# Performance work log

Measured on AMD Instinct MI355X. Metric: run time of the kernel, lower is better.

## Reference

```python
import jax, jax.numpy as jnp
import numpy as np

B, SEED, GEN = 32, 128, 384
IN, H, OUT = 171, 1024, 171


def setup_inputs() -> dict:
    key = jax.random.key(0)
    ks = jax.random.split(key, 16)
    s = 0.05
    w = lambda k, shape: (jax.random.normal(k, shape, jnp.float32) * s)
    inp = {
        "seed_seq": jax.random.normal(ks[0], (B, SEED, IN), jnp.float32),
        "Wih1": w(ks[1], (4 * H, IN)),  "Whh1": w(ks[2], (4 * H, H)),
        "bih1": w(ks[3], (4 * H,)),     "bhh1": w(ks[4], (4 * H,)),
        "Wih2": w(ks[5], (4 * H, H)),   "Whh2": w(ks[6], (4 * H, H)),
        "bih2": w(ks[7], (4 * H,)),     "bhh2": w(ks[8], (4 * H,)),
        "Wih3": w(ks[9], (4 * H, H)),   "Whh3": w(ks[10], (4 * H, H)),
        "bih3": w(ks[11], (4 * H,)),    "bhh3": w(ks[12], (4 * H,)),
        "Wdec": w(ks[13], (OUT, H)),    "bdec": w(ks[14], (OUT,)),
        "gen_len": GEN,
    }
    return inp


def _lstm_cell(x, h, c, Wih, Whh, bih, bhh):
    # PyTorch LSTMCell: gate order i, f, g, o
    gates = x @ Wih.T + bih + h @ Whh.T + bhh  # [B, 4H]
    i, f, g, o = jnp.split(gates, 4, axis=-1)
    c_new = jax.nn.sigmoid(f) * c + jax.nn.sigmoid(i) * jnp.tanh(g)
    h_new = jax.nn.sigmoid(o) * jnp.tanh(c_new)
    return h_new, c_new


def reference(seed_seq, Wih1, Whh1, bih1, bhh1, Wih2, Whh2, bih2, bhh2,
              Wih3, Whh3, bih3, bhh3, Wdec, bdec, gen_len):
    batch = seed_seq.shape[0]
    hsz = Whh1.shape[1]
    z = jnp.zeros((batch, hsz), seed_seq.dtype)

    def step(state, x):
        h1, c1, h2, c2, h3, c3 = state
        h1, c1 = _lstm_cell(x, h1, c1, Wih1, Whh1, bih1, bhh1)
        h2, c2 = _lstm_cell(h1, h2, c2, Wih2, Whh2, bih2, bhh2)
        h3, c3 = _lstm_cell(h2, h3, c3, Wih3, Whh3, bih3, bhh3)
        out = h3 @ Wdec.T + bdec
        return (h1, c1, h2, c2, h3, c3), out

    # conditioning (seed) phase: scan over time-major seed sequence
    state0 = (z, z, z, z, z, z)
    state, seed_outs = jax.lax.scan(step, state0, jnp.swapaxes(seed_seq, 0, 1))

    def gen_step(carry, _):
        cur, st = carry
        st, out = step(st, cur)
        return (out, st), out

    _, gen_outs = jax.lax.scan(gen_step, (seed_outs[-1], state), None, length=gen_len)

    outs = jnp.concatenate([seed_outs, gen_outs], axis=0)  # [T, B, OUT]
    return jnp.swapaxes(outs, 0, 1)  # [B, T, OUT]
```

## Files before the change

kernel.cpp:

```cpp
#include <hip/hip_runtime.h>
#include <hip/hip_bf16.h>
#include <math.h>

#define NB    32
#define NSEED 128
#define NTT   512
#define NIN   171
#define NINP  192
#define NH    1024
#define NG    4096
#define NOUT  171
#define NOUTP 176
#define NWG   256

typedef unsigned short u16;
typedef unsigned int u32;
typedef __attribute__((ext_vector_type(8))) short bf16x8;
typedef __attribute__((ext_vector_type(4))) float f32x4;

__device__ __host__ inline u16 f2bf(float x) {
  union { float f; unsigned u; } v; v.f = x;
  unsigned r = v.u + 0x7FFFu + ((v.u >> 16) & 1u);
  return (u16)(r >> 16);
}

__global__ void pack_mat(const float* __restrict__ src, u16* __restrict__ dst, int ktiles) {
  int id = blockIdx.x * 256 + threadIdx.x;
  int total = ktiles * 256 * 64;
  if (id >= total) return;
  int lane = id & 63;
  int nt = (id >> 6) & 255;
  int kt = id >> 14;
  int c = lane & 15, q = lane >> 4;
  int r = (c & 3) * 1024 + nt * 4 + (c >> 2);
  int K = ktiles * 32;
  const float* s = src + (size_t)r * K + kt * 32 + q * 8;
  __attribute__((aligned(16))) u16 o[8];
#pragma unroll
  for (int j = 0; j < 8; ++j) o[j] = f2bf(s[j]);
  *(bf16x8*)(dst + (size_t)id * 8) = *(const bf16x8*)o;
}

__global__ void pack_wih1(const float* __restrict__ src, u16* __restrict__ dst) {
  int id = blockIdx.x * 256 + threadIdx.x;
  if (id >= 6 * 256 * 64) return;
  int lane = id & 63;
  int nt = (id >> 6) & 255;
  int kt = id >> 14;
  int c = lane & 15, q = lane >> 4;
  int r = (c & 3) * 1024 + nt * 4 + (c >> 2);
  int k0 = kt * 32 + q * 8;
  __attribute__((aligned(16))) u16 o[8];
#pragma unroll
  for (int j = 0; j < 8; ++j) {
    int k = k0 + j;
    o[j] = (k < NIN) ? f2bf(src[(size_t)r * NIN + k]) : (u16)0;
  }
  *(bf16x8*)(dst + (size_t)id * 8) = *(const bf16x8*)o;
}

__global__ void pack_wdec(const float* __restrict__ src, u16* __restrict__ dst) {
  int id = blockIdx.x * 256 + threadIdx.x;
  if (id >= 32 * 11 * 64) return;
  int lane = id & 63;
  int nt = (id >> 6) % 11;
  int kt = (id >> 6) / 11;
  int c = lane & 15, q = lane >> 4;
  int r = nt * 16 + c;
  int k0 = kt * 32 + q * 8;
  __attribute__((aligned(16))) u16 o[8];
#pragma unroll
  for (int j = 0; j < 8; ++j) {
    o[j] = (r < NOUT) ? f2bf(src[(size_t)r * NH + k0 + j]) : (u16)0;
  }
  *(bf16x8*)(dst + (size_t)id * 8) = *(const bf16x8*)o;
}

__global__ void pack_seed(const float* __restrict__ src, u16* __restrict__ dst) {
  int id = blockIdx.x * 256 + threadIdx.x;
  if (id >= NSEED * NB * NINP) return;
  int kp = id % NINP;
  int b = (id / NINP) % NB;
  int t = id / (NINP * NB);
  float v = (kp < NIN) ? src[((size_t)b * NSEED + t) * NIN + kp] : 0.f;
  dst[id] = f2bf(v);
}

__global__ void wfuse_kernel(const float* __restrict__ wih1, const float* __restrict__ wdec,
                             float* __restrict__ tmp) {
  int n = blockIdx.x;
  int k = blockIdx.y * 256 + threadIdx.x;
  const float* wr = wih1 + (size_t)n * NIN;
  float s = 0.f;
  for (int i = 0; i < NIN; ++i) s += wr[i] * wdec[(size_t)i * NH + k];
  tmp[(size_t)n * NH + k] = s;
}

__global__ void prep_bias(const float* bih1, const float* bhh1, const float* bih2, const float* bhh2,
                          const float* bih3, const float* bhh3, const float* __restrict__ wih1,
                          const float* __restrict__ bdec_in,
                          float* b1s, float* b1g, float* b2, float* b3, float* bdecp,
                          int* __restrict__ flags) {
  int n = blockIdx.x * 256 + threadIdx.x;
  if (n >= NG) return;
  int wgi = n >> 4, c = n & 15;
  int r = (c & 3) * 1024 + wgi * 4 + (c >> 2);
  float v1 = bih1[r] + bhh1[r];
  b1s[n] = v1;
  float bf = 0.f;
  for (int i = 0; i < NIN; ++i) bf += wih1[(size_t)r * NIN + i] * bdec_in[i];
  b1g[n] = v1 + bf;
  b2[n] = bih2[r] + bhh2[r];
  b3[n] = bih3[r] + bhh3[r];
  if (n < NOUTP) bdecp[n] = (n < NOUT) ? bdec_in[n] : 0.f;
  if (n < NWG) flags[n] = 0;
}

__device__ __forceinline__ float fsig(float x) {
  return __builtin_amdgcn_rcpf(1.f + __expf(-x));
}
__device__ __forceinline__ float ftanh(float x) {
  return 1.f - 2.f * __builtin_amdgcn_rcpf(1.f + __expf(2.f * x));
}

#define MFMA_BF16 __builtin_amdgcn_mfma_f32_16x16x32_bf16

__device__ __forceinline__ void mm32_lds(f32x4& d0, f32x4& d1, const u16* wl,
                                         const u16* __restrict__ x, int wv, int lane) {
  int m = lane & 15, q = lane >> 4;
  const u16* xa = x + m * NH + q * 8 + wv * 32;
  const u16* xb = xa + 16 * NH;
  const u16* wb = wl + lane * 8;
  bf16x8 w[8], a0[8], a1[8];
#pragma unroll
  for (int i = 0; i < 8; ++i) w[i] = *(const bf16x8*)(wb + (size_t)(wv + 4 * i) * 512);
#pragma unroll
  for (int i = 0; i < 8; ++i) {
    a0[i] = *(const bf16x8*)(xa + i * 128);
    a1[i] = *(const bf16x8*)(xb + i * 128);
  }
#pragma unroll
  for (int i = 0; i < 8; ++i) {
    d0 = MFMA_BF16(a0[i], w[i], d0, 0, 0, 0);
    d1 = MFMA_BF16(a1[i], w[i], d1, 0, 0, 0);
  }
}

__device__ __forceinline__ void mm32_glb(f32x4& d0, f32x4& d1, const u16* __restrict__ wgb,
                                         const u16* __restrict__ x, int wv, int lane) {
  int m = lane & 15, q = lane >> 4;
  const u16* xa = x + m * NH + q * 8 + wv * 32;
  const u16* xb = xa + 16 * NH;
  const u16* wb = wgb + lane * 8;
  bf16x8 w[8], a0[8], a1[8];
#pragma unroll
  for (int i = 0; i < 8; ++i) w[i] = *(const bf16x8*)(wb + (size_t)(wv + 4 * i) * 131072);
#pragma unroll
  for (int i = 0; i < 8; ++i) {
    a0[i] = *(const bf16x8*)(xa + i * 128);
    a1[i] = *(const bf16x8*)(xb + i * 128);
  }
#pragma unroll
  for (int i = 0; i < 8; ++i) {
    d0 = MFMA_BF16(a0[i], w[i], d0, 0, 0, 0);
    d1 = MFMA_BF16(a1[i], w[i], d1, 0, 0, 0);
  }
}

__device__ __forceinline__ void mm6_glb(f32x4& d0, f32x4& d1, const u16* __restrict__ wbase,
                                        const u16* __restrict__ x, int wv, int lane) {
  int m = lane & 15, q = lane >> 4;
  const u16* xa = x + m * NINP + q * 8;
  const u16* xb = xa + 16 * NINP;
  const u16* wb = wbase + lane * 8;
#pragma unroll
  for (int i = 0; i < 2; ++i) {
    int kt = wv + 4 * i;
    if (kt >= 6) break;
    bf16x8 w = *(const bf16x8*)(wb + (size_t)kt * 131072);
    bf16x8 a0 = *(const bf16x8*)(xa + kt * 32);
    bf16x8 a1 = *(const bf16x8*)(xb + kt * 32);
    d0 = MFMA_BF16(a0, w, d0, 0, 0, 0);
    d1 = MFMA_BF16(a1, w, d1, 0, 0, 0);
  }
}

__global__ __launch_bounds__(256, 1) void lstm_main(
    const u16* __restrict__ whh1, const u16* __restrict__ whh2, const u16* __restrict__ whh3,
    const u16* __restrict__ wih2, const u16* __restrict__ wih3,
    const u16* __restrict__ wfuse, const u16* __restrict__ wih1,
    const u16* __restrict__ seedp,
    u16* __restrict__ h1h, u16* __restrict__ h2h, u16* __restrict__ h3h,
    const float* __restrict__ b1s, const float* __restrict__ b1g,
    const float* __restrict__ b2, const float* __restrict__ b3,
    int* __restrict__ flags)
{
  __shared__ u16  wlds[3 * 16384];
  __shared__ float red[4][64][8];
  __shared__ float gbuf[32][16];
  __shared__ float cst[3][32][4];

  int wg = blockIdx.x;
  int tid = threadIdx.x;
  int wv = tid >> 6, lane = tid & 63;

  {
    const u16* srcs[3] = { wih2 + (size_t)wg * 512, wih3 + (size_t)wg * 512,
                           wfuse + (size_t)wg * 512 };
#pragma unroll
    for (int m = 0; m < 3; ++m) {
      for (int i = tid; i < 2048; i += 256) {
        int kt = i >> 6, ln = i & 63;
        *(bf16x8*)&wlds[m * 16384 + (kt * 64 + ln) * 8] =
            *(const bf16x8*)(srcs[m] + ((size_t)kt * 16384 + ln) * 8);
      }
    }
    float* cp = &cst[0][0][0];
    for (int i = tid; i < 3 * 32 * 4; i += 256) cp[i] = 0.f;
  }
  __syncthreads();

  int c0 = tid & 15;
  float bv_s  = b1s[wg * 16 + c0];
  float bv_g  = b1g[wg * 16 + c0];
  float bv_2  = b2 [wg * 16 + c0];
  float bv_3  = b3 [wg * 16 + c0];

  const u16* whhg[3] = { whh1 + (size_t)wg * 512, whh2 + (size_t)wg * 512,
                         whh3 + (size_t)wg * 512 };
  const u16* wih1g = wih1 + (size_t)wg * 512;

  int ep = 0;
  for (int t = 0; t < NTT; ++t) {
    for (int l = 0; l < 3; ++l) {
      f32x4 d0 = {0.f, 0.f, 0.f, 0.f}, d1 = {0.f, 0.f, 0.f, 0.f};
      bool isseed = (t < NSEED);

      if (l == 0 && isseed)
        mm6_glb(d0, d1, wih1g, seedp + (size_t)t * NB * NINP, wv, lane);
      if (t > 0) {
        const u16* hs = (l == 0) ? h1h + (size_t)(t - 1) * NB * NH
                     : (l == 1) ? h2h + (size_t)(t - 1) * NB * NH
                                : h3h + (size_t)(t - 1) * NB * NH;
        mm32_glb(d0, d1, whhg[l], hs, wv, lane);
      }

      bool skipwait = (l == 0 && isseed);
      if (ep > 0 && !skipwait) {
        if (tid < 64) {
          const int* fp = flags + (tid << 2);
          for (;;) {
            int f0 = __hip_atomic_load(fp + 0, __ATOMIC_RELAXED, __HIP_MEMORY_SCOPE_AGENT);
            int f1 = __hip_atomic_load(fp + 1, __ATOMIC_RELAXED, __HIP_MEMORY_SCOPE_AGENT);
            int f2 = __hip_atomic_load(fp + 2, __ATOMIC_RELAXED, __HIP_MEMORY_SCOPE_AGENT);
            int f3 = __hip_atomic_load(fp + 3, __ATOMIC_RELAXED, __HIP_MEMORY_SCOPE_AGENT);
            int mn = min(min(f0, f1), min(f2, f3));
            if (__all(mn >= ep)) break;
            __builtin_amdgcn_s_sleep(1);
          }
        }
        __syncthreads();
      }

      if (l == 0) {
        if (!isseed)
          mm32_lds(d0, d1, &wlds[2 * 16384], h3h + (size_t)(t - 1) * NB * NH, wv, lane);
      } else {
        const u16* xs = (l == 1) ? h1h + (size_t)t * NB * NH
                                 : h2h + (size_t)t * NB * NH;
        mm32_lds(d0, d1, &wlds[(l - 1) * 16384], xs, wv, lane);
      }

#pragma unroll
      for (int r = 0; r < 4; ++r) { red[wv][lane][r] = d0[r]; red[wv][lane][4 + r] = d1[r]; }
      __syncthreads();
      {
        int c = tid & 15, brow = tid >> 4;
        float bv = (l == 0) ? (isseed ? bv_s : bv_g) : (l == 1) ? bv_2 : bv_3;
        int srcl = ((brow >> 2) << 4) | c;
#pragma unroll
        for (int mt = 0; mt < 2; ++mt) {
          int b = brow + mt * 16;
          int idx = mt * 4 + (brow & 3);
          gbuf[b][c] = red[0][srcl][idx] + red[1][srcl][idx] +
                       red[2][srcl][idx] + red[3][srcl][idx] + bv;
        }
      }
      __syncthreads();

      if (tid < 128) {
        int b = tid & 31, jl = tid >> 5;
        float gi = gbuf[b][jl * 4 + 0], gf = gbuf[b][jl * 4 + 1];
        float gg = gbuf[b][jl * 4 + 2], go = gbuf[b][jl * 4 + 3];
        float si = fsig(gi);
        float sf = fsig(gf);
        float so = fsig(go);
        float cn = sf * cst[l][b][jl] + si * ftanh(gg);
        cst[l][b][jl] = cn;
        float hn = so * ftanh(cn);
        unsigned hv = (unsigned)f2bf(hn);
        unsigned other = (unsigned)__shfl_xor((int)hv, 32, 64);
        if (lane < 32) {
          unsigned val = hv | (other << 16);
          int w01 = tid >> 6;
          u16* hdst = (l == 0) ? h1h + (size_t)t * NB * NH
                    : (l == 1) ? h2h + (size_t)t * NB * NH
                               : h3h + (size_t)t * NB * NH;
          u32* hp = (u32*)hdst + (size_t)b * 512 + wg * 2 + w01;
          __hip_atomic_store(hp, val, __ATOMIC_RELAXED, __HIP_MEMORY_SCOPE_AGENT);
        }
      }

      __syncthreads();
      ++ep;
      if (tid == 0)
        __hip_atomic_store(&flags[wg], ep, __ATOMIC_RELAXED, __HIP_MEMORY_SCOPE_AGENT);
    }
  }
}

__global__ __launch_bounds__(256) void dec_kernel(
    const u16* __restrict__ h3h, const u16* __restrict__ wdec,
    const float* __restrict__ bdecp, float* __restrict__ out)
{
  int task = blockIdx.x * 4 + (threadIdx.x >> 6);
  int lane = threadIdx.x & 63;
  int nt = task % 11, rt = task / 11;
  if (rt >= NTT) return;
  int m = lane & 15, q = lane >> 4;
  const u16* xa = h3h + ((size_t)rt * 32 + m) * NH + q * 8;
  const u16* xb = xa + (size_t)16 * NH;
  f32x4 d0 = {0.f, 0.f, 0.f, 0.f}, d1 = {0.f, 0.f, 0.f, 0.f};
  for (int kt = 0; kt < 32; ++kt) {
    bf16x8 bf = *(const bf16x8*)(wdec + ((size_t)(kt * 11 + nt) * 64 + lane) * 8);
    bf16x8 a0 = *(const bf16x8*)(xa + kt * 32);
    bf16x8 a1 = *(const bf16x8*)(xb + kt * 32);
    d0 = MFMA_BF16(a0, bf, d0, 0, 0, 0);
    d1 = MFMA_BF16(a1, bf, d1, 0, 0, 0);
  }
  int o = nt * 16 + m;
  if (o >= NOUT) return;
  float bv = bdecp[o];
#pragma unroll
  for (int reg = 0; reg < 4; ++reg) {
    int row0 = rt * 32 + q * 4 + reg;
    out[(((size_t)(row0 & 31)) * NTT + (row0 >> 5)) * NOUT + o] = d0[reg] + bv;
    int row1 = row0 + 16;
    out[(((size_t)(row1 & 31)) * NTT + (row1 >> 5)) * NOUT + o] = d1[reg] + bv;
  }
}

extern "C" void kernel_launch(void* const* d_in, const int* in_sizes, int n_in,
                              void* d_out, int out_size, void* d_ws, size_t ws_size,
                              hipStream_t stream) {
  const float* seed = (const float*)d_in[0];
  const float* Wih1 = (const float*)d_in[1];
  const float* Whh1 = (const float*)d_in[2];
  const float* bih1 = (const float*)d_in[3];
  const float* bhh1 = (const float*)d_in[4];
  const float* Wih2 = (const float*)d_in[5];
  const float* Whh2 = (const float*)d_in[6];
  const float* bih2 = (const float*)d_in[7];
  const float* bhh2 = (const float*)d_in[8];
  const float* Wih3 = (const float*)d_in[9];
  const float* Whh3 = (const float*)d_in[10];
  const float* bih3 = (const float*)d_in[11];
  const float* bhh3 = (const float*)d_in[12];
  const float* Wdec = (const float*)d_in[13];
  const float* bdec = (const float*)d_in[14];

  char* ws = (char*)d_ws;
  size_t off = 0;
  auto alloc = [&](size_t bytes) -> void* {
    void* p = ws + off;
    off += (bytes + 63) & ~(size_t)63;
    return p;
  };
  const size_t BIGPK = (size_t)32 * 256 * 64 * 8 * 2;
  const size_t HHIST = (size_t)NTT * NB * NH * 2;
  u16* whh1p  = (u16*)alloc(BIGPK);
  u16* whh2p  = (u16*)alloc(BIGPK);
  u16* whh3p  = (u16*)alloc(BIGPK);
  u16* wih2p  = (u16*)alloc(BIGPK);
  u16* wih3p  = (u16*)alloc(BIGPK);
  u16* wfusep = (u16*)alloc(BIGPK);
  u16* wih1p  = (u16*)alloc((size_t)6 * 256 * 64 * 8 * 2);
  u16* wdecp  = (u16*)alloc((size_t)32 * 11 * 64 * 8 * 2);
  u16* seedp  = (u16*)alloc((size_t)NSEED * NB * NINP * 2);
  u16* h1h    = (u16*)alloc(HHIST);
  u16* h2h    = (u16*)alloc(HHIST);
  u16* h3h    = (u16*)alloc(HHIST);
  float* b1s  = (float*)alloc((size_t)NG * 4);
  float* b1g  = (float*)alloc((size_t)NG * 4);
  float* b2   = (float*)alloc((size_t)NG * 4);
  float* b3   = (float*)alloc((size_t)NG * 4);
  float* bdecp = (float*)alloc((size_t)NOUTP * 4);
  int* flags  = (int*)alloc((size_t)NWG * 4);
  float* wftmp = (float*)h3h;

  pack_mat<<<dim3(2048), dim3(256), 0, stream>>>(Whh1, whh1p, 32);
  pack_mat<<<dim3(2048), dim3(256), 0, stream>>>(Whh2, whh2p, 32);
  pack_mat<<<dim3(2048), dim3(256), 0, stream>>>(Whh3, whh3p, 32);
  pack_mat<<<dim3(2048), dim3(256), 0, stream>>>(Wih2, wih2p, 32);
  pack_mat<<<dim3(2048), dim3(256), 0, stream>>>(Wih3, wih3p, 32);
  pack_wih1<<<dim3(384), dim3(256), 0, stream>>>(Wih1, wih1p);
  wfuse_kernel<<<dim3(4096, 4), dim3(256), 0, stream>>>(Wih1, Wdec, wftmp);
  pack_mat<<<dim3(2048), dim3(256), 0, stream>>>(wftmp, wfusep, 32);
  pack_wdec<<<dim3(88), dim3(256), 0, stream>>>(Wdec, wdecp);
  pack_seed<<<dim3(3072), dim3(256), 0, stream>>>(seed, seedp);
  prep_bias<<<dim3(16), dim3(256), 0, stream>>>(bih1, bhh1, bih2, bhh2, bih3, bhh3,
                                                Wih1, bdec, b1s, b1g, b2, b3, bdecp, flags);
  lstm_main<<<dim3(NWG), dim3(256), 0, stream>>>(
      whh1p, whh2p, whh3p, wih2p, wih3p, wfusep, wih1p, seedp,
      h1h, h2h, h3h, b1s, b1g, b2, b3, flags);
  dec_kernel<<<dim3(1408), dim3(256), 0, stream>>>(h3h, wdecp, bdecp, (float*)d_out);
}
```

Before: 7.976 ms.

## Use hierarchical group barrier and keep Whh1 slice resident in LDS

Replaces the flat grid barrier, where every workgroup polled all 256 flags, with a two-level scheme. A leader workgroup in each group of 32 polls its group's flags and publishes a 16-bit group flag, and every workgroup then polls the 8 group flags with a single uncached 16-byte load. This cuts polling traffic on the shared flags. It also caches each workgroup's Whh1 slice in LDS next to the other three weight blocks, so layer 1's recurrent matmul reads LDS instead of global memory. The costs are an extra hop of barrier latency through the leader, 16-bit epoch counters, and 128KB of LDS per workgroup.

```diff
diff --git a/kernel.cpp b/kernel.cpp
--- a/kernel.cpp
+++ b/kernel.cpp
@@ -17,6 +17,7 @@
 typedef unsigned int u32;
 typedef __attribute__((ext_vector_type(8))) short bf16x8;
 typedef __attribute__((ext_vector_type(4))) float f32x4;
+typedef __attribute__((ext_vector_type(4))) int i32x4;
 
 __device__ __host__ inline u16 f2bf(float x) {
   union { float f; unsigned u; } v; v.f = x;
@@ -100,7 +101,7 @@
                           const float* bih3, const float* bhh3, const float* __restrict__ wih1,
                           const float* __restrict__ bdec_in,
                           float* b1s, float* b1g, float* b2, float* b3, float* bdecp,
-                          int* __restrict__ flags) {
+                          int* __restrict__ flags, unsigned short* __restrict__ gflag) {
   int n = blockIdx.x * 256 + threadIdx.x;
   if (n >= NG) return;
   int wgi = n >> 4, c = n & 15;
@@ -114,6 +115,7 @@
   b3[n] = bih3[r] + bhh3[r];
   if (n < NOUTP) bdecp[n] = (n < NOUT) ? bdec_in[n] : 0.f;
   if (n < NWG) flags[n] = 0;
+  if (n < 8) gflag[n] = 0;
 }
 
 __device__ __forceinline__ float fsig(float x) {
@@ -193,9 +195,9 @@
     u16* __restrict__ h1h, u16* __restrict__ h2h, u16* __restrict__ h3h,
     const float* __restrict__ b1s, const float* __restrict__ b1g,
     const float* __restrict__ b2, const float* __restrict__ b3,
-    int* __restrict__ flags)
+    int* __restrict__ flags, unsigned short* __restrict__ gflag)
 {
-  __shared__ u16  wlds[3 * 16384];
+  __shared__ u16  wlds[4 * 16384];
   __shared__ float red[4][64][8];
   __shared__ float gbuf[32][16];
   __shared__ float cst[3][32][4];
@@ -203,12 +205,15 @@
   int wg = blockIdx.x;
   int tid = threadIdx.x;
   int wv = tid >> 6, lane = tid & 63;
+  int grp = wg >> 5;
+  bool islead = (wg & 31) == 0;
+  int grpbase = wg & ~31;
 
   {
-    const u16* srcs[3] = { wih2 + (size_t)wg * 512, wih3 + (size_t)wg * 512,
-                           wfuse + (size_t)wg * 512 };
-#pragma unroll
-    for (int m = 0; m < 3; ++m) {
+    const u16* srcs[4] = { wih2 + (size_t)wg * 512, wih3 + (size_t)wg * 512,
+                           wfuse + (size_t)wg * 512, whh1 + (size_t)wg * 512 };
+#pragma unroll
+    for (int m = 0; m < 4; ++m) {
       for (int i = tid; i < 2048; i += 256) {
         int kt = i >> 6, ln = i & 63;
         *(bf16x8*)&wlds[m * 16384 + (kt * 64 + ln) * 8] =
@@ -226,8 +231,8 @@
   float bv_2  = b2 [wg * 16 + c0];
   float bv_3  = b3 [wg * 16 + c0];
 
-  const u16* whhg[3] = { whh1 + (size_t)wg * 512, whh2 + (size_t)wg * 512,
-                         whh3 + (size_t)wg * 512 };
+  const u16* whh2g = whh2 + (size_t)wg * 512;
+  const u16* whh3g = whh3 + (size_t)wg * 512;
   const u16* wih1g = wih1 + (size_t)wg * 512;
 
   int ep = 0;
@@ -239,23 +244,39 @@
       if (l == 0 && isseed)
         mm6_glb(d0, d1, wih1g, seedp + (size_t)t * NB * NINP, wv, lane);
       if (t > 0) {
-        const u16* hs = (l == 0) ? h1h + (size_t)(t - 1) * NB * NH
-                     : (l == 1) ? h2h + (size_t)(t - 1) * NB * NH
-                                : h3h + (size_t)(t - 1) * NB * NH;
-        mm32_glb(d0, d1, whhg[l], hs, wv, lane);
+        if (l == 0)
+          mm32_lds(d0, d1, &wlds[3 * 16384], h1h + (size_t)(t - 1) * NB * NH, wv, lane);
+        else if (l == 1)
+          mm32_glb(d0, d1, whh2g, h2h + (size_t)(t - 1) * NB * NH, wv, lane);
+        else
+          mm32_glb(d0, d1, whh3g, h3h + (size_t)(t - 1) * NB * NH, wv, lane);
       }
 
       bool skipwait = (l == 0 && isseed);
       if (ep > 0 && !skipwait) {
         if (tid < 64) {
-          const int* fp = flags + (tid << 2);
+          if (islead) {
+            const int* fp = flags + grpbase;
+            for (;;) {
+              int f = (tid < 32)
+                  ? __hip_atomic_load(fp + tid, __ATOMIC_RELAXED, __HIP_MEMORY_SCOPE_AGENT)
+                  : ep;
+              if (__all(f >= ep)) break;
+              __builtin_amdgcn_s_sleep(1);
+            }
+            if (tid == 0)
+              __hip_atomic_store(gflag + grp, (unsigned short)ep,
+                                 __ATOMIC_RELAXED, __HIP_MEMORY_SCOPE_AGENT);
+          }
           for (;;) {
-            int f0 = __hip_atomic_load(fp + 0, __ATOMIC_RELAXED, __HIP_MEMORY_SCOPE_AGENT);
-            int f1 = __hip_atomic_load(fp + 1, __ATOMIC_RELAXED, __HIP_MEMORY_SCOPE_AGENT);
-            int f2 = __hip_atomic_load(fp + 2, __ATOMIC_RELAXED, __HIP_MEMORY_SCOPE_AGENT);
-            int f3 = __hip_atomic_load(fp + 3, __ATOMIC_RELAXED, __HIP_MEMORY_SCOPE_AGENT);
-            int mn = min(min(f0, f1), min(f2, f3));
-            if (__all(mn >= ep)) break;
+            i32x4 g;
+            asm volatile("global_load_dwordx4 %0, %1, off sc0 sc1\n\ts_waitcnt vmcnt(0)"
+                         : "=v"(g) : "v"(gflag) : "memory");
+            unsigned m0 = min(min((unsigned)(g.x & 0xFFFF), ((unsigned)g.x) >> 16),
+                              min((unsigned)(g.y & 0xFFFF), ((unsigned)g.y) >> 16));
+            unsigned m1 = min(min((unsigned)(g.z & 0xFFFF), ((unsigned)g.z) >> 16),
+                              min((unsigned)(g.w & 0xFFFF), ((unsigned)g.w) >> 16));
+            if (min(m0, m1) >= (unsigned)ep) break;
             __builtin_amdgcn_s_sleep(1);
           }
         }
@@ -396,6 +417,7 @@
   float* b3   = (float*)alloc((size_t)NG * 4);
   float* bdecp = (float*)alloc((size_t)NOUTP * 4);
   int* flags  = (int*)alloc((size_t)NWG * 4);
+  unsigned short* gflag = (unsigned short*)alloc(64);
   float* wftmp = (float*)h3h;
 
   pack_mat<<<dim3(2048), dim3(256), 0, stream>>>(Whh1, whh1p, 32);
@@ -409,9 +431,10 @@
   pack_wdec<<<dim3(88), dim3(256), 0, stream>>>(Wdec, wdecp);
   pack_seed<<<dim3(3072), dim3(256), 0, stream>>>(seed, seedp);
   prep_bias<<<dim3(16), dim3(256), 0, stream>>>(bih1, bhh1, bih2, bhh2, bih3, bhh3,
-                                                Wih1, bdec, b1s, b1g, b2, b3, bdecp, flags);
+                                                Wih1, bdec, b1s, b1g, b2, b3, bdecp,
+                                                flags, gflag);
   lstm_main<<<dim3(NWG), dim3(256), 0, stream>>>(
       whh1p, whh2p, whh3p, wih2p, wih3p, wfusep, wih1p, seedp,
-      h1h, h2h, h3h, b1s, b1g, b2, b3, flags);
+      h1h, h2h, h3h, b1s, b1g, b2, b3, flags, gflag);
   dec_kernel<<<dim3(1408), dim3(256), 0, stream>>>(h3h, wdecp, bdecp, (float*)d_out);
 }
```

Result: slower. 10.93 ms (+37.1%).

## Cache Whh1 in LDS, fuse gate reduction into one wave, tighten flag spin

Applied to the files above, without the earlier changes.

Whh1 is now staged into LDS alongside the other resident weights, so the layer-1 recurrent matmul reads LDS instead of global memory. The gate reduction and cell update are merged into a single wave at raised priority, which removes a barrier and the gbuf staging. That wave publishes its flag right after its own h store drains, instead of waiting for a block-wide sync. The flag spin now runs on wave 1 only, using a cache-bypassing dwordx4 inline-asm load. Activation loads are also reordered ahead of weight loads. This trades more LDS use and some inline-asm memory-ordering assumptions for a shorter per-layer critical path.

```diff
diff --git a/kernel.cpp b/kernel.cpp
--- a/kernel.cpp
+++ b/kernel.cpp
@@ -17,6 +17,7 @@
 typedef unsigned int u32;
 typedef __attribute__((ext_vector_type(8))) short bf16x8;
 typedef __attribute__((ext_vector_type(4))) float f32x4;
+typedef __attribute__((ext_vector_type(4))) int i32x4;
 
 __device__ __host__ inline u16 f2bf(float x) {
   union { float f; unsigned u; } v; v.f = x;
@@ -133,12 +134,12 @@
   const u16* wb = wl + lane * 8;
   bf16x8 w[8], a0[8], a1[8];
 #pragma unroll
-  for (int i = 0; i < 8; ++i) w[i] = *(const bf16x8*)(wb + (size_t)(wv + 4 * i) * 512);
-#pragma unroll
   for (int i = 0; i < 8; ++i) {
     a0[i] = *(const bf16x8*)(xa + i * 128);
     a1[i] = *(const bf16x8*)(xb + i * 128);
   }
+#pragma unroll
+  for (int i = 0; i < 8; ++i) w[i] = *(const bf16x8*)(wb + (size_t)(wv + 4 * i) * 512);
 #pragma unroll
   for (int i = 0; i < 8; ++i) {
     d0 = MFMA_BF16(a0[i], w[i], d0, 0, 0, 0);
@@ -154,12 +155,12 @@
   const u16* wb = wgb + lane * 8;
   bf16x8 w[8], a0[8], a1[8];
 #pragma unroll
-  for (int i = 0; i < 8; ++i) w[i] = *(const bf16x8*)(wb + (size_t)(wv + 4 * i) * 131072);
-#pragma unroll
   for (int i = 0; i < 8; ++i) {
     a0[i] = *(const bf16x8*)(xa + i * 128);
     a1[i] = *(const bf16x8*)(xb + i * 128);
   }
+#pragma unroll
+  for (int i = 0; i < 8; ++i) w[i] = *(const bf16x8*)(wb + (size_t)(wv + 4 * i) * 131072);
 #pragma unroll
   for (int i = 0; i < 8; ++i) {
     d0 = MFMA_BF16(a0[i], w[i], d0, 0, 0, 0);
@@ -195,9 +196,9 @@
     const float* __restrict__ b2, const float* __restrict__ b3,
     int* __restrict__ flags)
 {
-  __shared__ u16  wlds[3 * 16384];
+  __shared__ u16  wlds[4 * 16384];
   __shared__ float red[4][64][8];
-  __shared__ float gbuf[32][16];
+  __shared__ float biasLds[4][16];
   __shared__ float cst[3][32][4];
 
   int wg = blockIdx.x;
@@ -205,10 +206,10 @@
   int wv = tid >> 6, lane = tid & 63;
 
   {
-    const u16* srcs[3] = { wih2 + (size_t)wg * 512, wih3 + (size_t)wg * 512,
-                           wfuse + (size_t)wg * 512 };
-#pragma unroll
-    for (int m = 0; m < 3; ++m) {
+    const u16* srcs[4] = { wih2 + (size_t)wg * 512, wih3 + (size_t)wg * 512,
+                           wfuse + (size_t)wg * 512, whh1 + (size_t)wg * 512 };
+#pragma unroll
+    for (int m = 0; m < 4; ++m) {
       for (int i = tid; i < 2048; i += 256) {
         int kt = i >> 6, ln = i & 63;
         *(bf16x8*)&wlds[m * 16384 + (kt * 64 + ln) * 8] =
@@ -217,17 +218,16 @@
     }
     float* cp = &cst[0][0][0];
     for (int i = tid; i < 3 * 32 * 4; i += 256) cp[i] = 0.f;
+    if (tid < 64) {
+      int row = tid >> 4, c = tid & 15;
+      const float* src = (row == 0) ? b1s : (row == 1) ? b1g : (row == 2) ? b2 : b3;
+      biasLds[row][c] = src[wg * 16 + c];
+    }
   }
   __syncthreads();
 
-  int c0 = tid & 15;
-  float bv_s  = b1s[wg * 16 + c0];
-  float bv_g  = b1g[wg * 16 + c0];
-  float bv_2  = b2 [wg * 16 + c0];
-  float bv_3  = b3 [wg * 16 + c0];
-
-  const u16* whhg[3] = { whh1 + (size_t)wg * 512, whh2 + (size_t)wg * 512,
-                         whh3 + (size_t)wg * 512 };
+  const u16* whh2g = whh2 + (size_t)wg * 512;
+  const u16* whh3g = whh3 + (size_t)wg * 512;
   const u16* wih1g = wih1 + (size_t)wg * 512;
 
   int ep = 0;
@@ -239,28 +239,27 @@
       if (l == 0 && isseed)
         mm6_glb(d0, d1, wih1g, seedp + (size_t)t * NB * NINP, wv, lane);
       if (t > 0) {
-        const u16* hs = (l == 0) ? h1h + (size_t)(t - 1) * NB * NH
-                     : (l == 1) ? h2h + (size_t)(t - 1) * NB * NH
-                                : h3h + (size_t)(t - 1) * NB * NH;
-        mm32_glb(d0, d1, whhg[l], hs, wv, lane);
+        if (l == 0)
+          mm32_lds(d0, d1, &wlds[3 * 16384], h1h + (size_t)(t - 1) * NB * NH, wv, lane);
+        else if (l == 1)
+          mm32_glb(d0, d1, whh2g, h2h + (size_t)(t - 1) * NB * NH, wv, lane);
+        else
+          mm32_glb(d0, d1, whh3g, h3h + (size_t)(t - 1) * NB * NH, wv, lane);
       }
 
       bool skipwait = (l == 0 && isseed);
-      if (ep > 0 && !skipwait) {
-        if (tid < 64) {
-          const int* fp = flags + (tid << 2);
-          for (;;) {
-            int f0 = __hip_atomic_load(fp + 0, __ATOMIC_RELAXED, __HIP_MEMORY_SCOPE_AGENT);
-            int f1 = __hip_atomic_load(fp + 1, __ATOMIC_RELAXED, __HIP_MEMORY_SCOPE_AGENT);
-            int f2 = __hip_atomic_load(fp + 2, __ATOMIC_RELAXED, __HIP_MEMORY_SCOPE_AGENT);
-            int f3 = __hip_atomic_load(fp + 3, __ATOMIC_RELAXED, __HIP_MEMORY_SCOPE_AGENT);
-            int mn = min(min(f0, f1), min(f2, f3));
-            if (__all(mn >= ep)) break;
-            __builtin_amdgcn_s_sleep(1);
-          }
+      if (ep > 0 && !skipwait && wv == 1) {
+        const int* fp = flags + (lane << 2);
+        for (;;) {
+          i32x4 f;
+          asm volatile("global_load_dwordx4 %0, %1, off sc0 sc1\n\ts_waitcnt vmcnt(0)"
+                       : "=v"(f) : "v"(fp) : "memory");
+          int mn = min(min(f.x, f.y), min(f.z, f.w));
+          if (__all(mn >= ep)) break;
+          __builtin_amdgcn_s_sleep(1);
         }
-        __syncthreads();
       }
+      __syncthreads();
 
       if (l == 0) {
         if (!isseed)
@@ -274,47 +273,49 @@
 #pragma unroll
       for (int r = 0; r < 4; ++r) { red[wv][lane][r] = d0[r]; red[wv][lane][4 + r] = d1[r]; }
       __syncthreads();
-      {
-        int c = tid & 15, brow = tid >> 4;
-        float bv = (l == 0) ? (isseed ? bv_s : bv_g) : (l == 1) ? bv_2 : bv_3;
-        int srcl = ((brow >> 2) << 4) | c;
-#pragma unroll
-        for (int mt = 0; mt < 2; ++mt) {
-          int b = brow + mt * 16;
-          int idx = mt * 4 + (brow & 3);
-          gbuf[b][c] = red[0][srcl][idx] + red[1][srcl][idx] +
-                       red[2][srcl][idx] + red[3][srcl][idx] + bv;
+
+      int epn = ep + 1;
+      if (tid < 64) {
+        __builtin_amdgcn_s_setprio(1);
+        int b = tid & 31, upair = tid >> 5;
+        int srcl_base = ((b & 15) >> 2) << 4;
+        int idx = ((b >> 4) << 2) | (b & 3);
+        int bsel = (l == 0) ? (isseed ? 0 : 1) : (l + 1);
+        float g[8];
+#pragma unroll
+        for (int u2 = 0; u2 < 2; ++u2) {
+          int u = upair * 2 + u2;
+#pragma unroll
+          for (int gi = 0; gi < 4; ++gi) {
+            int c = u * 4 + gi;
+            int srcl = srcl_base | c;
+            g[u2 * 4 + gi] = red[0][srcl][idx] + red[1][srcl][idx] +
+                             red[2][srcl][idx] + red[3][srcl][idx] + biasLds[bsel][c];
+          }
         }
+        unsigned hv[2];
+#pragma unroll
+        for (int u2 = 0; u2 < 2; ++u2) {
+          int u = upair * 2 + u2;
+          float si = fsig(g[u2 * 4 + 0]);
+          float sf = fsig(g[u2 * 4 + 1]);
+          float so = fsig(g[u2 * 4 + 3]);
+          float cn = sf * cst[l][b][u] + si * ftanh(g[u2 * 4 + 2]);
+          cst[l][b][u] = cn;
+          hv[u2] = (unsigned)f2bf(so * ftanh(cn));
+        }
+        unsigned val = hv[0] | (hv[1] << 16);
+        u16* hdst = (l == 0) ? h1h + (size_t)t * NB * NH
+                  : (l == 1) ? h2h + (size_t)t * NB * NH
+                             : h3h + (size_t)t * NB * NH;
+        u32* hp = (u32*)hdst + (size_t)b * 512 + wg * 2 + upair;
+        __hip_atomic_store(hp, val, __ATOMIC_RELAXED, __HIP_MEMORY_SCOPE_AGENT);
+        asm volatile("s_waitcnt vmcnt(0)" ::: "memory");
+        if (tid == 0)
+          __hip_atomic_store(&flags[wg], epn, __ATOMIC_RELAXED, __HIP_MEMORY_SCOPE_AGENT);
+        __builtin_amdgcn_s_setprio(0);
       }
-      __syncthreads();
-
-      if (tid < 128) {
-        int b = tid & 31, jl = tid >> 5;
-        float gi = gbuf[b][jl * 4 + 0], gf = gbuf[b][jl * 4 + 1];
-        float gg = gbuf[b][jl * 4 + 2], go = gbuf[b][jl * 4 + 3];
-        float si = fsig(gi);
-        float sf = fsig(gf);
-        float so = fsig(go);
-        float cn = sf * cst[l][b][jl] + si * ftanh(gg);
-        cst[l][b][jl] = cn;
-        float hn = so * ftanh(cn);
-        unsigned hv = (unsigned)f2bf(hn);
-        unsigned other = (unsigned)__shfl_xor((int)hv, 32, 64);
-        if (lane < 32) {
-          unsigned val = hv | (other << 16);
-          int w01 = tid >> 6;
-          u16* hdst = (l == 0) ? h1h + (size_t)t * NB * NH
-                    : (l == 1) ? h2h + (size_t)t * NB * NH
-                               : h3h + (size_t)t * NB * NH;
-          u32* hp = (u32*)hdst + (size_t)b * 512 + wg * 2 + w01;
-          __hip_atomic_store(hp, val, __ATOMIC_RELAXED, __HIP_MEMORY_SCOPE_AGENT);
-        }
-      }
-
-      __syncthreads();
-      ++ep;
-      if (tid == 0)
-        __hip_atomic_store(&flags[wg], ep, __ATOMIC_RELAXED, __HIP_MEMORY_SCOPE_AGENT);
+      ep = epn;
     }
   }
 }
```

Measured after the change: 6.708 ms, median of 3. -15.9%, faster.
